# Optimization experiments

Hardware: AMD Instinct MI355X
Metric: run time of the kernel (lower is better)

Reference implementation:

```python
import jax, jax.numpy as jnp
import numpy as np
import math

B, N, D, K = 8, 2048, 1024, 128
PI = math.pi


def setup_inputs() -> dict:
    key = jax.random.key(0)
    ks = jax.random.split(key, 4)
    x = jax.random.normal(ks[0], (B, N, D), dtype=jnp.float32)
    W_proj = jax.random.normal(ks[1], (D, 6 * K), dtype=jnp.float32) * (D ** -0.5)
    # structured bias init as in OscillatorProjection._init_weights
    b = np.zeros(6 * K, np.float32)
    groups = [K // 4, K // 2, K - K // 4 - K // 2]
    centers = [0.3, 0.65, 0.97]
    off = 3 * K
    for n_k, c in zip(groups, centers):
        b[off:off + n_k] = math.log(c / (1.0 - c))
        off += n_k
    b[4 * K:5 * K] = math.log(0.65 / 0.35)
    b[5 * K:] = -2.0
    b_proj = jnp.asarray(b)
    omega_base = jnp.exp(jnp.linspace(math.log(2.0 * PI / N), math.log(PI * (1.0 - 1.0 / K)), K)).astype(jnp.float32)
    W_phase = jax.random.normal(ks[2], (D, K), dtype=jnp.float32) * 0.001
    b_phase = jnp.zeros((K,), jnp.float32)
    W_res = jax.random.normal(ks[3], (4 * K - 2, D), dtype=jnp.float32) * 0.002
    lambda_pcg = jnp.float32(0.5)
    res_scale = jnp.float32(0.05)
    return dict(x=x, W_proj=W_proj, b_proj=b_proj, omega_base=omega_base,
                W_phase=W_phase, b_phase=b_phase, W_res=W_res,
                lambda_pcg=lambda_pcg, res_scale=res_scale)


def _resonance_scan(alpha, drive):
    # linear recurrence r_t = alpha_t * r_{t-1} + d_t, r_0 = 0, along axis=1
    def combine(e1, e2):
        a1, b1 = e1
        a2, b2 = e2
        return (a2 * a1, a2 * b1 + b2)
    _, r = jax.lax.associative_scan(combine, (alpha, drive), axis=1)
    return r


def reference(x, W_proj, b_proj, omega_base, W_phase, b_phase, W_res, lambda_pcg, res_scale):
    _, n, _ = x.shape
    out = x @ W_proj + b_proj  # [B, n, 6K]
    A_r, Om_r, Ph_r, Ga_r, Go_r, Be_r = jnp.split(out, 6, axis=-1)
    A = jnp.minimum(jax.nn.softplus(A_r), 3.0)
    omega = jnp.clip(jax.nn.sigmoid(Om_r) * PI + omega_base, 1e-4, PI - 1e-4)
    phi = jnp.tanh(Ph_r) * PI
    alpha = jax.nn.sigmoid(Ga_r)
    g_out = jax.nn.sigmoid(Go_r)
    beta = jax.nn.sigmoid(Be_r)
    positions = jnp.log1p(jnp.arange(n, dtype=jnp.float32)).reshape(1, n, 1)
    angle = omega * positions + phi
    cos_a = jnp.cos(angle)
    sin_a = jnp.sin(angle)
    drive = (1.0 - alpha) * A
    # fused real/imag scan sharing alpha (mirrors the fused Triton path)
    r = _resonance_scan(jnp.concatenate([alpha, alpha], axis=-1),
                        jnp.concatenate([drive * cos_a, drive * sin_a], axis=-1))
    r_r, r_i = r[..., :K], r[..., K:]
    readout = r_r * cos_a + r_i * sin_a
    r_r = r_r - beta * readout * cos_a
    r_i = r_i - beta * readout * sin_a
    # state norm: rescale only when |r| > 1
    modulus = jnp.sqrt(r_r ** 2 + r_i ** 2 + 1e-8)
    scale = jnp.maximum(modulus, 1.0)
    r_r = r_r / scale
    r_i = r_i / scale
    # rotate into the oscillator frame
    rho_re = r_r * cos_a + r_i * sin_a
    rho_im = -r_r * sin_a + r_i * cos_a
    rho_norm = jnp.sqrt(rho_re ** 2 + rho_im ** 2 + 1e-6)
    pq = x @ W_phase + b_phase
    align = (rho_re * jnp.cos(pq) + rho_im * jnp.sin(pq)) / rho_norm
    gate = jax.nn.sigmoid(lambda_pcg * align)
    rho_re = gate * rho_re
    rho_im = gate * rho_im
    # SCPM: adjacent-oscillator complex cross products -> 4K-2 features
    cross_re = rho_re[..., :-1] * rho_re[..., 1:] + rho_im[..., :-1] * rho_im[..., 1:]
    cross_im = rho_im[..., :-1] * rho_re[..., 1:] - rho_re[..., :-1] * rho_im[..., 1:]
    feats = jnp.concatenate([g_out * rho_re, g_out * rho_im, cross_re, cross_im], axis=-1)
    return x + res_scale * (feats @ W_res)
```

## Files before the change

### kernel.cpp

```cpp
#include <hip/hip_runtime.h>
#include <math.h>

#define PI_F 3.14159265358979323846f
#define SEG 256
#define SLEN 8
typedef unsigned short u16;
typedef __attribute__((ext_vector_type(8))) short bf16x8;
typedef __attribute__((ext_vector_type(4))) float f32x4;

__device__ __forceinline__ float sigmoidf_(float x){ return __fdividef(1.0f, 1.0f+__expf(-x)); }
__device__ __forceinline__ float softplusf_(float x){
    return fmaxf(x, 0.f) + __logf(1.f + __expf(-fabsf(x)));
}
__device__ __forceinline__ float tanhpi_(float x){
    float t = __expf(-2.f*fabsf(x));
    float th = __fdividef(1.f - t, 1.f + t);
    return copysignf(th, x)*PI_F;
}
__device__ __forceinline__ void fsincos(float a, float* s, float* c){
    float r = a * 0.15915494309189535f;
    r = r - floorf(r);
#if __has_builtin(__builtin_amdgcn_sinf)
    *s = __builtin_amdgcn_sinf(r);
    *c = __builtin_amdgcn_cosf(r);
#else
    float t = r * 6.283185307179586f;
    *s = __sinf(t); *c = __cosf(t);
#endif
}
__device__ __forceinline__ u16 f2bf(float f){
    unsigned u = __float_as_uint(f);
    return (u16)((u + 0x7FFFu + ((u>>16)&1u)) >> 16);
}
__device__ __forceinline__ float b2f(u16 v){
    return __uint_as_float(((unsigned)v)<<16);
}
__device__ __forceinline__ void gl_lds16(const u16* g, u16* l){
    __builtin_amdgcn_global_load_lds((const __attribute__((address_space(1))) void*)g,
                                     (__attribute__((address_space(3))) void*)l, 16, 0, 0);
}

__global__ __launch_bounds__(256) void k_cvt_x(const float* __restrict__ x, u16* __restrict__ xb){
    size_t i = ((size_t)blockIdx.x*256 + threadIdx.x)*8;
    float4 v0 = *(const float4*)&x[i];
    float4 v1 = *(const float4*)&x[i+4];
    ushort4 a = make_ushort4(f2bf(v0.x),f2bf(v0.y),f2bf(v0.z),f2bf(v0.w));
    ushort4 b = make_ushort4(f2bf(v1.x),f2bf(v1.y),f2bf(v1.z),f2bf(v1.w));
    *(ushort4*)&xb[i]   = a;
    *(ushort4*)&xb[i+4] = b;
}

__global__ __launch_bounds__(256) void k_tcvt(const float* __restrict__ W, u16* __restrict__ Wt,
                                              int K, int Ns, int KD){
    __shared__ float s[32][33];
    const int tx = threadIdx.x & 31, ty = threadIdx.x >> 5;
    const int k0 = blockIdx.y*32, n0 = blockIdx.x*32;
    #pragma unroll
    for (int i=0;i<4;i++){
        int k = k0 + ty + i*8;
        s[ty+i*8][tx] = (k < K) ? W[(size_t)k*Ns + n0 + tx] : 0.f;
    }
    __syncthreads();
    #pragma unroll
    for (int i=0;i<4;i++){
        int n = n0 + ty + i*8;
        Wt[(size_t)n*KD + k0 + tx] = f2bf(s[tx][ty+i*8]);
    }
}

__global__ __launch_bounds__(256,2) void k_mm1(
    const u16* __restrict__ A,
    const u16* __restrict__ Bt,
    const float* __restrict__ bp, const float* __restrict__ bph,
    u16* __restrict__ C)
{
    __shared__ u16 sm[3*12288];
    const int bid = blockIdx.x;
    const int swz = (bid & 7)*56 + (bid >> 3);
    const int by = swz / 7, bx = swz - by*7;
    const int r0 = by*256, c0 = bx*128;
    const int tid = threadIdx.x;
    const int w = tid >> 6, lane = tid & 63;
    const int wm = w >> 1, wn = w & 1;
    const int lr = lane & 15, lk = lane >> 4;

    const int cg = ((lane&3) ^ ((lane>>3)&3))*8;
    const u16* gA = A  + (size_t)(r0 + w*16 + (lane>>2))*1024 + cg;
    const u16* gB = Bt + (size_t)(c0 + w*16 + (lane>>2))*1024 + cg;
    const int ldsA = w*512;
    const int ldsB = 8192 + w*512;

    const int cs = (lk ^ ((lr>>1)&3))*8;
    const int aoff = (wm*128 + lr)*32 + cs;
    const int boff = 8192 + (wn*64 + lr)*32 + cs;

    f32x4 acc[8][4] = {};

    #pragma unroll
    for (int t=0;t<2;t++){
        #pragma unroll
        for (int j=0;j<4;j++)
            gl_lds16(gA + j*64*1024 + t*32, sm + t*12288 + ldsA + j*2048);
        #pragma unroll
        for (int j=0;j<2;j++)
            gl_lds16(gB + j*64*1024 + t*32, sm + t*12288 + ldsB + j*2048);
    }
    asm volatile("s_waitcnt vmcnt(6)" ::: "memory");
    __builtin_amdgcn_s_barrier();
    __builtin_amdgcn_sched_barrier(0);

    for (int k=0; k<32; ++k){
        const u16* bufp = sm + (k%3)*12288;
        u16*       bufn = sm + ((k+2)%3)*12288;
        const int  k0n  = (k+2)*32;
        bf16x8 af[8], bfr[4];

        if (k < 30){
            #pragma unroll
            for (int j=0;j<4;j++)
                gl_lds16(gA + j*64*1024 + k0n, bufn + ldsA + j*2048);
            #pragma unroll
            for (int j=0;j<2;j++)
                gl_lds16(gB + j*64*1024 + k0n, bufn + ldsB + j*2048);
        }
        af[0] = *(const bf16x8*)&bufp[aoff];
        #pragma unroll
        for (int n=0;n<4;n++) bfr[n] = *(const bf16x8*)&bufp[boff + n*512];
        #pragma unroll
        for (int m=1;m<8;m++) af[m]  = *(const bf16x8*)&bufp[aoff + m*512];

        __builtin_amdgcn_s_setprio(1);
        #pragma unroll
        for (int m=0;m<8;m++)
            #pragma unroll
            for (int n=0;n<4;n++)
                acc[m][n] = __builtin_amdgcn_mfma_f32_16x16x32_bf16(af[m], bfr[n], acc[m][n],0,0,0);
        __builtin_amdgcn_s_setprio(0);

        if (k < 30)       asm volatile("s_waitcnt vmcnt(6)" ::: "memory");
        else if (k == 30) asm volatile("s_waitcnt vmcnt(0)" ::: "memory");
        __builtin_amdgcn_s_barrier();
        __builtin_amdgcn_sched_barrier(0);
    }

    #pragma unroll
    for (int n=0;n<4;n++){
        const int col = c0 + wn*64 + n*16 + lr;
        const float bl = (col < 768) ? bp[col] : bph[col-768];
        #pragma unroll
        for (int m=0;m<8;m++){
            const int row = r0 + wm*128 + m*16 + lk*4;
            #pragma unroll
            for (int r=0;r<4;r++)
                C[(size_t)(row+r)*896 + col] = f2bf(acc[m][n][r] + bl);
        }
    }
}

__global__ __launch_bounds__(256) void k_mm2(
    const u16* __restrict__ A,
    const u16* __restrict__ Bt,
    const u16* __restrict__ Xb,
    const float* __restrict__ rs_p,
    float* __restrict__ O)
{
    const int bid = blockIdx.x;
    const int swz = (bid & 7)*128 + (bid >> 3);
    const int by = swz >> 3, bx = swz & 7;

    __shared__ u16 As[128*32];
    __shared__ u16 Bs[128*32];
    const int tid = threadIdx.x;
    const int w = tid>>6, lane = tid&63;
    const int wm = w>>1, wn = w&1;
    const int r0 = by*128, c0 = bx*128;

    const int cg = ((lane&3) ^ ((lane>>3)&3))*8;
    const u16* ga[2]; const u16* gb[2]; u16 *la[2], *lb[2];
    #pragma unroll
    for (int i=0;i<2;i++){
        ga[i] = A  + (size_t)(r0 + w*32 + i*16 + (lane>>2))*512 + cg;
        gb[i] = Bt + (size_t)(c0 + w*32 + i*16 + (lane>>2))*512 + cg;
        la[i] = As + w*1024 + i*512;
        lb[i] = Bs + w*1024 + i*512;
    }
    const int lr = lane&15, lk = lane>>4;
    const int cs = (lk ^ ((lr>>1)&3))*8;
    const int ao = (wm*64 + lr)*32 + cs;
    const int bo = (wn*64 + lr)*32 + cs;

    f32x4 acc[4][4] = {};
    for (int k0=0; k0<512; k0+=32){
        gl_lds16(ga[0]+k0, la[0]); gl_lds16(ga[1]+k0, la[1]);
        gl_lds16(gb[0]+k0, lb[0]); gl_lds16(gb[1]+k0, lb[1]);
        __syncthreads();
        bf16x8 af[4], bfr[4];
        #pragma unroll
        for (int m=0;m<4;m++) af[m]  = *(const bf16x8*)&As[ao + m*512];
        #pragma unroll
        for (int n=0;n<4;n++) bfr[n] = *(const bf16x8*)&Bs[bo + n*512];
        #pragma unroll
        for (int m=0;m<4;m++)
            #pragma unroll
            for (int n=0;n<4;n++)
                acc[m][n] = __builtin_amdgcn_mfma_f32_16x16x32_bf16(af[m], bfr[n], acc[m][n], 0,0,0);
        __syncthreads();
    }
    const float rs = rs_p[0];
    #pragma unroll
    for (int n=0;n<4;n++){
        int col = c0 + wn*64 + n*16 + lr;
        #pragma unroll
        for (int m=0;m<4;m++){
            int row = r0 + wm*64 + m*16 + lk*4;
            #pragma unroll
            for (int r=0;r<4;r++){
                size_t idx = (size_t)(row+r)*1024 + col;
                O[idx] = b2f(Xb[idx]) + rs*acc[m][n][r];
            }
        }
    }
}

__global__ __launch_bounds__(128) void k_s1(
    const u16* __restrict__ C1,
    const float* __restrict__ omega_base,
    float* __restrict__ Ag, float* __restrict__ Br, float* __restrict__ Bi)
{
    const int k = threadIdx.x;
    const int seg = blockIdx.x, b = blockIdx.y;
    const float ob = omega_base[k];
    const int n0 = seg*SLEN;
    float aag = 1.f, br = 0.f, bi = 0.f;
    #pragma unroll 4
    for (int s=0; s<SLEN; s++){
        const int n = n0 + s;
        const u16* row = C1 + (size_t)(b*2048+n)*896;
        float Ar = b2f(row[k]);
        float Om = b2f(row[128+k]);
        float Ph = b2f(row[256+k]);
        float Ga = b2f(row[384+k]);
        float alpha = sigmoidf_(Ga);
        float A = fminf(softplusf_(Ar), 3.0f);
        float omega = fminf(fmaxf(sigmoidf_(Om)*PI_F + ob, 1e-4f), PI_F-1e-4f);
        float phi = tanhpi_(Ph);
        float pos = __logf(1.f + (float)n);
        float sa, ca; fsincos(fmaf(omega, pos, phi), &sa, &ca);
        float drive = (1.f-alpha)*A;
        aag *= alpha;
        br = fmaf(alpha, br, drive*ca);
        bi = fmaf(alpha, bi, drive*sa);
    }
    const size_t o = (size_t)(b*SEG + seg)*128 + k;
    Ag[o] = aag; Br[o] = br; Bi[o] = bi;
}

__global__ __launch_bounds__(256) void k_s2(
    const float* __restrict__ Ag, const float* __restrict__ Br, const float* __restrict__ Bi,
    float* __restrict__ Pr, float* __restrict__ Pi)
{
    const int gid = blockIdx.x*256 + threadIdx.x;
    const int b = gid >> 7, k = gid & 127;
    float pr = 0.f, pi = 0.f;
    #pragma unroll 8
    for (int seg=0; seg<SEG; seg++){
        const size_t o = (size_t)(b*SEG + seg)*128 + k;
        float a = Ag[o], r = Br[o], i = Bi[o];
        Pr[o] = pr; Pi[o] = pi;
        pr = fmaf(a, pr, r);
        pi = fmaf(a, pi, i);
    }
}

__global__ __launch_bounds__(128) void k_s3(
    const u16* __restrict__ C1,
    const float* __restrict__ omega_base,
    const float* __restrict__ lam_p,
    const float* __restrict__ Pr, const float* __restrict__ Pi,
    u16* __restrict__ F)
{
    const int k = threadIdx.x;
    const int seg = blockIdx.x, b = blockIdx.y;
    const float ob = omega_base[k];
    const float lam = lam_p[0];
    __shared__ float sre[2][129], sim[2][129];

    const size_t po = (size_t)(b*SEG + seg)*128 + k;
    float rr = Pr[po], ri = Pi[po];
    const int n0 = seg*SLEN;

    #pragma unroll 2
    for (int s=0; s<SLEN; s++){
        const int n = n0 + s;
        const u16* row = C1 + (size_t)(b*2048+n)*896;
        float Ar = b2f(row[k]);
        float Om = b2f(row[128+k]);
        float Ph = b2f(row[256+k]);
        float Ga = b2f(row[384+k]);
        float Go = b2f(row[512+k]);
        float Be = b2f(row[640+k]);
        float pq = b2f(row[768+k]);
        float alpha = sigmoidf_(Ga);
        float A = fminf(softplusf_(Ar), 3.0f);
        float omega = fminf(fmaxf(sigmoidf_(Om)*PI_F + ob, 1e-4f), PI_F-1e-4f);
        float phi = tanhpi_(Ph);
        float pos = __logf(1.f + (float)n);
        float sa, ca; fsincos(fmaf(omega, pos, phi), &sa, &ca);
        float drive = (1.f-alpha)*A;
        rr = fmaf(alpha, rr, drive*ca);
        ri = fmaf(alpha, ri, drive*sa);
        float readout = rr*ca + ri*sa;
        float beta = sigmoidf_(Be);
        float r2r = rr - beta*readout*ca;
        float r2i = ri - beta*readout*sa;
        float m2 = r2r*r2r + r2i*r2i + 1e-8f;
        float inv = fminf(rsqrtf(m2), 1.0f);
        r2r *= inv; r2i *= inv;
        float rho_re =  r2r*ca + r2i*sa;
        float rho_im = -r2r*sa + r2i*ca;
        float rho2 = rho_re*rho_re + rho_im*rho_im + 1e-6f;
        float spq, cpq; fsincos(pq, &spq, &cpq);
        float align = (rho_re*cpq + rho_im*spq)*rsqrtf(rho2);
        float gate = sigmoidf_(lam*align);
        rho_re *= gate; rho_im *= gate;
        float go = sigmoidf_(Go);

        const int buf = s & 1;
        sre[buf][k] = rho_re; sim[buf][k] = rho_im;
        __syncthreads();

        u16* frow = F + (size_t)(b*2048+n)*512;
        frow[k]       = f2bf(go*rho_re);
        frow[128 + k] = f2bf(go*rho_im);
        if (k < 127){
            float nre = sre[buf][k+1], nim = sim[buf][k+1];
            frow[256 + k] = f2bf(rho_re*nre + rho_im*nim);
            frow[383 + k] = f2bf(rho_im*nre - rho_re*nim);
        } else {
            frow[510] = 0; frow[511] = 0;
        }
    }
}

extern "C" void kernel_launch(void* const* d_in, const int* in_sizes, int n_in,
                              void* d_out, int out_size, void* d_ws, size_t ws_size,
                              hipStream_t stream)
{
    const float* x   = (const float*)d_in[0];
    const float* Wp  = (const float*)d_in[1];
    const float* bp  = (const float*)d_in[2];
    const float* ob  = (const float*)d_in[3];
    const float* Wph = (const float*)d_in[4];
    const float* bph = (const float*)d_in[5];
    const float* Wr  = (const float*)d_in[6];
    const float* lam = (const float*)d_in[7];
    const float* rs  = (const float*)d_in[8];
    float* out = (float*)d_out;

    char* ws = (char*)d_ws;
    u16*   C1  = (u16*)  (ws + 0);
    float* Ag  = (float*)(ws + 29360128);
    float* Brr = (float*)(ws + 30408704);
    float* Bii = (float*)(ws + 31457280);
    float* Pr  = (float*)(ws + 32505856);
    float* Pi  = (float*)(ws + 33554432);
    u16*   F   = (u16*)  (ws + 34603008);
    u16*   Wt  = (u16*)  (ws + 51380224);
    u16*   Wrt = (u16*)  (ws + 53215232);
    u16*   Xb  = (u16*)  (ws + 58720256);

    dim3 blk(256);
    hipLaunchKernelGGL(k_cvt_x, dim3(8192),   blk, 0, stream, x, Xb);
    hipLaunchKernelGGL(k_tcvt,  dim3(24,32),  blk, 0, stream, Wp,  Wt,            1024, 768,  1024);
    hipLaunchKernelGGL(k_tcvt,  dim3(4,32),   blk, 0, stream, Wph, Wt + 768*1024, 1024, 128,  1024);
    hipLaunchKernelGGL(k_tcvt,  dim3(32,16),  blk, 0, stream, Wr,  Wrt,           510,  1024, 512);
    hipLaunchKernelGGL(k_mm1,   dim3(448),    blk, 0, stream, Xb, Wt, bp, bph, C1);
    hipLaunchKernelGGL(k_s1,    dim3(SEG,8),  dim3(128), 0, stream, C1, ob, Ag, Brr, Bii);
    hipLaunchKernelGGL(k_s2,    dim3(4),      blk, 0, stream, Ag, Brr, Bii, Pr, Pi);
    hipLaunchKernelGGL(k_s3,    dim3(SEG,8),  dim3(128), 0, stream, C1, ob, lam, Pr, Pi, F);
    hipLaunchKernelGGL(k_mm2,   dim3(1024),   blk, 0, stream, F, Wrt, Xb, rs, out);
}
```

Before: 135.0 us.

## Triple-buffer LDS in output GEMM with prefetch distance two

Restructures the k_mm2 output projection GEMM main loop to use three LDS buffers, prefetching tiles two iterations ahead via direct global-to-LDS loads with explicit vmcnt waits and a single barrier per iteration. This replaces the load-sync-compute-sync pattern, so global memory latency overlaps with MFMA work. It also raises wave priority around the MFMA block. LDS usage triples to 48KB per block, which may reduce occupancy, and correctness depends on the hand-placed waitcnt counts.

```diff
diff --git a/kernel.cpp b/kernel.cpp
--- a/kernel.cpp
+++ b/kernel.cpp
@@ -164,48 +164,73 @@
     const float* __restrict__ rs_p,
     float* __restrict__ O)
 {
+    __shared__ u16 sm[3*8192];
     const int bid = blockIdx.x;
     const int swz = (bid & 7)*128 + (bid >> 3);
     const int by = swz >> 3, bx = swz & 7;
-
-    __shared__ u16 As[128*32];
-    __shared__ u16 Bs[128*32];
+    const int r0 = by*128, c0 = bx*128;
     const int tid = threadIdx.x;
     const int w = tid>>6, lane = tid&63;
     const int wm = w>>1, wn = w&1;
-    const int r0 = by*128, c0 = bx*128;
+    const int lr = lane&15, lk = lane>>4;
 
     const int cg = ((lane&3) ^ ((lane>>3)&3))*8;
-    const u16* ga[2]; const u16* gb[2]; u16 *la[2], *lb[2];
-    #pragma unroll
-    for (int i=0;i<2;i++){
-        ga[i] = A  + (size_t)(r0 + w*32 + i*16 + (lane>>2))*512 + cg;
-        gb[i] = Bt + (size_t)(c0 + w*32 + i*16 + (lane>>2))*512 + cg;
-        la[i] = As + w*1024 + i*512;
-        lb[i] = Bs + w*1024 + i*512;
-    }
-    const int lr = lane&15, lk = lane>>4;
+    const u16* gA = A  + (size_t)(r0 + w*32 + (lane>>2))*512 + cg;
+    const u16* gB = Bt + (size_t)(c0 + w*32 + (lane>>2))*512 + cg;
+    const int ldsA = w*1024;
+    const int ldsB = 4096 + w*1024;
+
     const int cs = (lk ^ ((lr>>1)&3))*8;
-    const int ao = (wm*64 + lr)*32 + cs;
-    const int bo = (wn*64 + lr)*32 + cs;
+    const int aoff = (wm*64 + lr)*32 + cs;
+    const int boff = 4096 + (wn*64 + lr)*32 + cs;
 
     f32x4 acc[4][4] = {};
-    for (int k0=0; k0<512; k0+=32){
-        gl_lds16(ga[0]+k0, la[0]); gl_lds16(ga[1]+k0, la[1]);
-        gl_lds16(gb[0]+k0, lb[0]); gl_lds16(gb[1]+k0, lb[1]);
-        __syncthreads();
+
+    #pragma unroll
+    for (int t=0;t<2;t++){
+        #pragma unroll
+        for (int i=0;i<2;i++){
+            gl_lds16(gA + i*16*512 + t*32, sm + t*8192 + ldsA + i*512);
+            gl_lds16(gB + i*16*512 + t*32, sm + t*8192 + ldsB + i*512);
+        }
+    }
+    asm volatile("s_waitcnt vmcnt(4)" ::: "memory");
+    __builtin_amdgcn_s_barrier();
+    __builtin_amdgcn_sched_barrier(0);
+
+    for (int k=0; k<16; ++k){
+        const u16* bufp = sm + (k%3)*8192;
+        u16*       bufn = sm + ((k+2)%3)*8192;
+        const int  k0n  = (k+2)*32;
         bf16x8 af[4], bfr[4];
-        #pragma unroll
-        for (int m=0;m<4;m++) af[m]  = *(const bf16x8*)&As[ao + m*512];
-        #pragma unroll
-        for (int n=0;n<4;n++) bfr[n] = *(const bf16x8*)&Bs[bo + n*512];
+
+        if (k < 14){
+            #pragma unroll
+            for (int i=0;i<2;i++){
+                gl_lds16(gA + i*16*512 + k0n, bufn + ldsA + i*512);
+                gl_lds16(gB + i*16*512 + k0n, bufn + ldsB + i*512);
+            }
+        }
+        af[0] = *(const bf16x8*)&bufp[aoff];
+        #pragma unroll
+        for (int n=0;n<4;n++) bfr[n] = *(const bf16x8*)&bufp[boff + n*512];
+        #pragma unroll
+        for (int m=1;m<4;m++) af[m]  = *(const bf16x8*)&bufp[aoff + m*512];
+
+        __builtin_amdgcn_s_setprio(1);
         #pragma unroll
         for (int m=0;m<4;m++)
             #pragma unroll
             for (int n=0;n<4;n++)
-                acc[m][n] = __builtin_amdgcn_mfma_f32_16x16x32_bf16(af[m], bfr[n], acc[m][n], 0,0,0);
-        __syncthreads();
-    }
+                acc[m][n] = __builtin_amdgcn_mfma_f32_16x16x32_bf16(af[m], bfr[n], acc[m][n],0,0,0);
+        __builtin_amdgcn_s_setprio(0);
+
+        if (k < 14)       asm volatile("s_waitcnt vmcnt(4)" ::: "memory");
+        else if (k == 14) asm volatile("s_waitcnt vmcnt(0)" ::: "memory");
+        __builtin_amdgcn_s_barrier();
+        __builtin_amdgcn_sched_barrier(0);
+    }
+
     const float rs = rs_p[0];
     #pragma unroll
     for (int n=0;n<4;n++){
```

Result: no change. 132.5 us (-1.9%).
